# Performance work log

Hardware: AMD Instinct MI355X
Metric: run time of the kernel (lower is better)

The kernel has to match this reference:

```python
import jax, jax.numpy as jnp
import numpy as np

B, P, K, HE, HF = 256, 128, 512, 1024, 512
D = K + HE + 2 * HF  # 2560, MLP input dim
HID = 64


def setup_inputs() -> dict:
    key = jax.random.key(0)
    ks = jax.random.split(key, 6)
    query = jax.random.normal(ks[0], (B, 1, HE), dtype=jnp.float32)
    keys = jax.random.normal(ks[1], (B, P, K), dtype=jnp.float32)
    frameLSTM_h = jax.random.normal(ks[2], (B, 1, 2 * HF), dtype=jnp.float32)
    mask = jax.random.randint(ks[3], (B, P), 0, 2, dtype=jnp.int32)
    mask = mask.at[:, 0].set(1)  # guarantee at least one unmasked player per row
    W1 = jax.random.normal(ks[4], (D, HID), dtype=jnp.float32) / np.float32(np.sqrt(D))
    W2 = jax.random.normal(ks[5], (HID, 1), dtype=jnp.float32) / np.float32(np.sqrt(HID))
    return dict(query=query, keys=keys, frameLSTM_h=frameLSTM_h, mask=mask, W1=W1, W2=W2)


def reference(query, keys, frameLSTM_h, mask, W1, W2):
    # Faithful to: cat([keys, query.repeat, frame.repeat]) @ W1 -> ReLU -> @ W2.
    # The pre-activation is linear, so splitting W1 by row-blocks is exactly the
    # same math without materializing the repeated/concatenated (B,P,D) tensor.
    W1k = W1[:K]            # (K, 64)
    W1q = W1[K:K + HE]      # (HE, 64)
    W1f = W1[K + HE:]       # (2*HF, 64)
    h = jax.nn.relu(
        jnp.einsum('bpk,kh->bph', keys, W1k)
        + jnp.einsum('boe,eh->boh', query, W1q)        # broadcasts over P
        + jnp.einsum('bof,fh->boh', frameLSTM_h, W1f)  # broadcasts over P
    )  # (B, P, 64)
    raw_scores = jnp.einsum('bph,ho->bp', h, W2)  # (B, P)
    raw_scores = jnp.where(mask == 0, -jnp.inf, raw_scores)
    weights = jax.nn.softmax(raw_scores, axis=1)  # (B, P)
    context = jnp.einsum('bp,bpk->bk', weights, keys)[:, None, :]  # (B, 1, K)
    embeddings = jnp.concatenate([context, frameLSTM_h], axis=2)   # (B, 1, K+2*HF)
    return embeddings, weights
```

## Files before the change

### kernel.cpp

```cpp
#include <hip/hip_runtime.h>
#include <hip/hip_bf16.h>
#include <cstdint>
#include <math.h>


typedef __bf16 bf16;
typedef __attribute__((ext_vector_type(8))) __bf16 bf16x8;
typedef __attribute__((ext_vector_type(4))) __bf16 bf16x4;
typedef __attribute__((ext_vector_type(4))) float f32x4;

#define NB 256
#define NP 128
#define NK 512
#define SKLD 520
#define K1_SK_BYTES (64 * SKLD * 2)
#define K1_SMEM (K1_SK_BYTES + 64*4 + 64*4)

__global__ __launch_bounds__(256) void prep_kernel(
    const float* __restrict__ query, const float* __restrict__ frame,
    const float* __restrict__ W1, bf16* __restrict__ w1kt,
    float* __restrict__ proj_part)
{
    const int blk = blockIdx.x;
    const int t = threadIdx.x;
    if (blk < 1024) {
        __shared__ float part[4][64];
        const int b = blk >> 2;
        const int q4 = blk & 3;
        const int h = t & 63;
        const int g = t >> 6;
        const float* src = (q4 < 2 ? query : frame) + (size_t)b * 1024 + (q4 & 1) * 512 + g * 128;
        const float* wrow = W1 + (size_t)(512 + q4 * 512 + g * 128) * 64 + h;
        float acc = 0.f;
#pragma unroll 8
        for (int dd = 0; dd < 128; dd++)
            acc += src[dd] * wrow[(size_t)dd * 64];
        part[g][h] = acc;
        __syncthreads();
        if (t < 64)
            proj_part[((size_t)q4 * NB + b) * 64 + t] =
                part[0][t] + part[1][t] + part[2][t] + part[3][t];
    } else {
        __shared__ float s[32][65];
        const int j = blk - 1024;
        const int k0 = j * 32;
#pragma unroll
        for (int i = 0; i < 8; i++) {
            const int idx = t + 256 * i;
            const int k = idx >> 6, h = idx & 63;
            s[k][h] = W1[(size_t)(k0 + k) * 64 + h];
        }
        __syncthreads();
#pragma unroll
        for (int i = 0; i < 8; i++) {
            const int idx = t + 256 * i;
            const int h = idx >> 5, kk = idx & 31;
            w1kt[(size_t)h * 512 + k0 + kk] = (bf16)s[kk][h];
        }
    }
}

__global__ __launch_bounds__(256, 2) void k1_scores(
    const float* __restrict__ keys, const float* __restrict__ W2,
    const bf16* __restrict__ w1kt, const float* __restrict__ proj_part,
    float* __restrict__ scores_ws)
{
    extern __shared__ char smem[];
    bf16* sk     = (bf16*)smem;
    float* projl = (float*)(smem + K1_SK_BYTES);
    float* w2l   = projl + 64;

    const int b    = blockIdx.x >> 1;
    const int half = blockIdx.x & 1;
    const int t = threadIdx.x;

    if (t < 64)
        projl[t] = proj_part[(size_t)b * 64 + t]
                 + proj_part[((size_t)NB + b) * 64 + t]
                 + proj_part[((size_t)2 * NB + b) * 64 + t]
                 + proj_part[((size_t)3 * NB + b) * 64 + t];
    else if (t < 128) w2l[t - 64] = W2[t - 64];

    const float* kb = keys + (size_t)b * (NP * NK) + (size_t)half * 64 * NK;
    {
        const int rowadd = (t >> 7);
        const int c0 = (t & 127) * 4;
#pragma unroll 8
        for (int i = 0; i < 32; i++) {
            const float4 v = *(const float4*)(kb + (size_t)i * 1024 + t * 4);
            bf16x4 bv;
            bv[0] = (bf16)v.x; bv[1] = (bf16)v.y; bv[2] = (bf16)v.z; bv[3] = (bf16)v.w;
            *(bf16x4*)(sk + (2 * i + rowadd) * SKLD + c0) = bv;
        }
    }
    __syncthreads();

    const int w = t >> 6;
    const int lane = t & 63;
    const int m = lane & 15;
    const int q = lane >> 4;

    const bf16* bbase = w1kt + (size_t)m * 512 + q * 8;
    bf16x8 Bc[4], Bn[4];
#pragma unroll
    for (int nt = 0; nt < 4; nt++) Bc[nt] = *(const bf16x8*)(bbase + nt * 8192);
#pragma unroll
    for (int nt = 0; nt < 4; nt++) Bn[nt] = *(const bf16x8*)(bbase + nt * 8192 + 32);

    f32x4 acc[4];
#pragma unroll
    for (int nt = 0; nt < 4; nt++) acc[nt] = (f32x4){0.f, 0.f, 0.f, 0.f};

#pragma unroll
    for (int kk = 0; kk < 16; kk++) {
        const bf16x8 A = *(const bf16x8*)(sk + (w * 16 + m) * SKLD + kk * 32 + q * 8);
        bf16x8 Bf[4];
#pragma unroll
        for (int nt = 0; nt < 4; nt++) Bf[nt] = Bc[nt];
#pragma unroll
        for (int nt = 0; nt < 4; nt++) Bc[nt] = Bn[nt];
        if (kk < 14) {
#pragma unroll
            for (int nt = 0; nt < 4; nt++)
                Bn[nt] = *(const bf16x8*)(bbase + nt * 8192 + (kk + 2) * 32);
        }
#pragma unroll
        for (int nt = 0; nt < 4; nt++)
            acc[nt] = __builtin_amdgcn_mfma_f32_16x16x32_bf16(A, Bf[nt], acc[nt], 0, 0, 0);
    }

    float pr[4] = {0.f, 0.f, 0.f, 0.f};
#pragma unroll
    for (int nt = 0; nt < 4; nt++) {
        const int h = nt * 16 + m;
        const float pv = projl[h];
        const float wv = w2l[h];
#pragma unroll
        for (int r = 0; r < 4; r++)
            pr[r] += fmaxf(acc[nt][r] + pv, 0.f) * wv;
    }
#pragma unroll
    for (int off = 1; off < 16; off <<= 1) {
#pragma unroll
        for (int r = 0; r < 4; r++) pr[r] += __shfl_xor(pr[r], off);
    }
    if (m == 0) {
        const int base = b * 128 + half * 64 + w * 16 + q * 4;
#pragma unroll
        for (int r = 0; r < 4; r++) scores_ws[base + r] = pr[r];
    }
}

__global__ __launch_bounds__(512) void k2_context(
    const float* __restrict__ keys, const float* __restrict__ frame,
    const int* __restrict__ mask, const float* __restrict__ scores_ws,
    float* __restrict__ out)
{
    __shared__ float s_sc[128];
    __shared__ float s_w[128];
    __shared__ float part[512];

    const int b = blockIdx.x;
    const int t = threadIdx.x;

    if (t < 128) {
        const float raw = scores_ws[b * 128 + t];
        s_sc[t] = (mask[b * 128 + t] == 0) ? -INFINITY : raw;
    }
    __syncthreads();

    if (t < 64) {
        float s0 = s_sc[t], s1 = s_sc[t + 64];
        float mx = fmaxf(s0, s1);
#pragma unroll
        for (int off = 32; off; off >>= 1) mx = fmaxf(mx, __shfl_xor(mx, off));
        float e0 = __expf(s0 - mx), e1 = __expf(s1 - mx);
        float sum = e0 + e1;
#pragma unroll
        for (int off = 32; off; off >>= 1) sum += __shfl_xor(sum, off);
        const float inv = 1.0f / sum;
        s_w[t] = e0 * inv;
        s_w[t + 64] = e1 * inv;
    }
    __syncthreads();

    if (t < 128) out[(size_t)NB * 1536 + b * 128 + t] = s_w[t];

    const int tg = t >> 8;
    const int tc = t & 255;
    const float* kb = keys + (size_t)b * (NP * NK);
    float a0 = 0.f, a1 = 0.f;
#pragma unroll 8
    for (int i = 0; i < 64; i++) {
        const int p = tg * 64 + i;
        const float wv = s_w[p];
        const float2 v = *(const float2*)(kb + (size_t)p * 512 + 2 * tc);
        a0 += wv * v.x;
        a1 += wv * v.y;
    }
    if (tg == 1) {
        part[2 * tc] = a0;
        part[2 * tc + 1] = a1;
    }
    __syncthreads();
    if (tg == 0) {
        out[(size_t)b * 1536 + 2 * tc]     = a0 + part[2 * tc];
        out[(size_t)b * 1536 + 2 * tc + 1] = a1 + part[2 * tc + 1];
    }

    out[(size_t)b * 1536 + 512 + t] = frame[(size_t)b * 1024 + t];
    out[(size_t)b * 1536 + 1024 + t] = frame[(size_t)b * 1024 + 512 + t];
}

extern "C" void kernel_launch(void* const* d_in, const int* in_sizes, int n_in,
                              void* d_out, int out_size, void* d_ws, size_t ws_size,
                              hipStream_t stream) {
    const float* query = (const float*)d_in[0];
    const float* keys  = (const float*)d_in[1];
    const float* frame = (const float*)d_in[2];
    const int*   mask  = (const int*)d_in[3];
    const float* W1    = (const float*)d_in[4];
    const float* W2    = (const float*)d_in[5];
    float* out = (float*)d_out;

    bf16*  w1kt      = (bf16*)d_ws;
    float* proj_part = (float*)((char*)d_ws + (64 << 10));
    float* scores_ws = (float*)((char*)d_ws + (320 << 10));

    hipFuncSetAttribute((const void*)k1_scores,
                        hipFuncAttributeMaxDynamicSharedMemorySize, K1_SMEM);

    prep_kernel<<<1040, 256, 0, stream>>>(query, frame, W1, w1kt, proj_part);
    k1_scores<<<512, 256, K1_SMEM, stream>>>(keys, W2, w1kt, proj_part, scores_ws);
    k2_context<<<256, 512, 0, stream>>>(keys, frame, mask, scores_ws, out);
}
```

Before: 138.3 us.

## Fuse context kernel into score kernel with per-batch inter-block flag handshake

```diff
diff --git a/kernel.cpp b/kernel.cpp
--- a/kernel.cpp
+++ b/kernel.cpp
@@ -14,12 +14,13 @@
 #define NK 512
 #define SKLD 520
 #define K1_SK_BYTES (64 * SKLD * 2)
-#define K1_SMEM (K1_SK_BYTES + 64*4 + 64*4)
+#define K1_SMEM (K1_SK_BYTES + 64*4 + 64*4 + 128*4)
 
 __global__ __launch_bounds__(256) void prep_kernel(
     const float* __restrict__ query, const float* __restrict__ frame,
     const float* __restrict__ W1, bf16* __restrict__ w1kt,
-    float* __restrict__ proj_part)
+    float* __restrict__ proj_part, int* __restrict__ flags,
+    float* __restrict__ out)
 {
     const int blk = blockIdx.x;
     const int t = threadIdx.x;
@@ -50,6 +51,13 @@
             const int k = idx >> 6, h = idx & 63;
             s[k][h] = W1[(size_t)(k0 + k) * 64 + h];
         }
+        if (j == 0) flags[t] = 0;
+#pragma unroll
+        for (int bb = 0; bb < 16; bb++) {
+            const int b = j * 16 + bb;
+            out[(size_t)b * 1536 + t] = 0.f;
+            out[(size_t)b * 1536 + 256 + t] = 0.f;
+        }
         __syncthreads();
 #pragma unroll
         for (int i = 0; i < 8; i++) {
@@ -60,15 +68,18 @@
     }
 }
 
-__global__ __launch_bounds__(256, 2) void k1_scores(
-    const float* __restrict__ keys, const float* __restrict__ W2,
+__global__ __launch_bounds__(256, 2) void k1_attn(
+    const float* __restrict__ keys, const float* __restrict__ frame,
+    const int* __restrict__ mask, const float* __restrict__ W2,
     const bf16* __restrict__ w1kt, const float* __restrict__ proj_part,
-    float* __restrict__ scores_ws)
+    float* __restrict__ scores_ws, int* __restrict__ flags,
+    float* __restrict__ out)
 {
     extern __shared__ char smem[];
     bf16* sk     = (bf16*)smem;
     float* projl = (float*)(smem + K1_SK_BYTES);
     float* w2l   = projl + 64;
+    float* wts   = w2l + 64;
 
     const int b    = blockIdx.x >> 1;
     const int half = blockIdx.x & 1;
@@ -83,7 +94,7 @@
 
     const float* kb = keys + (size_t)b * (NP * NK) + (size_t)half * 64 * NK;
     {
-        const int rowadd = (t >> 7);
+        const int rowadd = t >> 7;
         const int c0 = (t & 127) * 4;
 #pragma unroll 8
         for (int i = 0; i < 32; i++) {
@@ -147,30 +158,29 @@
     if (m == 0) {
         const int base = b * 128 + half * 64 + w * 16 + q * 4;
 #pragma unroll
-        for (int r = 0; r < 4; r++) scores_ws[base + r] = pr[r];
-    }
-}
-
-__global__ __launch_bounds__(512) void k2_context(
-    const float* __restrict__ keys, const float* __restrict__ frame,
-    const int* __restrict__ mask, const float* __restrict__ scores_ws,
-    float* __restrict__ out)
-{
-    __shared__ float s_sc[128];
-    __shared__ float s_w[128];
-    __shared__ float part[512];
-
-    const int b = blockIdx.x;
-    const int t = threadIdx.x;
+        for (int r = 0; r < 4; r++)
+            __hip_atomic_store(&scores_ws[base + r], pr[r],
+                               __ATOMIC_RELAXED, __HIP_MEMORY_SCOPE_AGENT);
+    }
+    __threadfence();
+    __syncthreads();
+
+    if (t == 0) {
+        atomicAdd(&flags[b], 1);
+        while (__hip_atomic_load(&flags[b], __ATOMIC_ACQUIRE,
+                                 __HIP_MEMORY_SCOPE_AGENT) < 2)
+            __builtin_amdgcn_s_sleep(1);
+    }
+    __syncthreads();
 
     if (t < 128) {
-        const float raw = scores_ws[b * 128 + t];
-        s_sc[t] = (mask[b * 128 + t] == 0) ? -INFINITY : raw;
-    }
-    __syncthreads();
-
-    if (t < 64) {
-        float s0 = s_sc[t], s1 = s_sc[t + 64];
+        const float raw = __hip_atomic_load(&scores_ws[b * 128 + t],
+                                            __ATOMIC_RELAXED, __HIP_MEMORY_SCOPE_AGENT);
+        wts[t] = (mask[b * 128 + t] == 0) ? -INFINITY : raw;
+    }
+    __syncthreads();
+    if (w == 0) {
+        float s0 = wts[lane], s1 = wts[lane + 64];
         float mx = fmaxf(s0, s1);
 #pragma unroll
         for (int off = 32; off; off >>= 1) mx = fmaxf(mx, __shfl_xor(mx, off));
@@ -179,37 +189,32 @@
 #pragma unroll
         for (int off = 32; off; off >>= 1) sum += __shfl_xor(sum, off);
         const float inv = 1.0f / sum;
-        s_w[t] = e0 * inv;
-        s_w[t + 64] = e1 * inv;
-    }
-    __syncthreads();
-
-    if (t < 128) out[(size_t)NB * 1536 + b * 128 + t] = s_w[t];
-
-    const int tg = t >> 8;
-    const int tc = t & 255;
-    const float* kb = keys + (size_t)b * (NP * NK);
-    float a0 = 0.f, a1 = 0.f;
+        wts[lane] = e0 * inv;
+        wts[lane + 64] = e1 * inv;
+    }
+    __syncthreads();
+
+    if (half == 0 && t < 128)
+        out[(size_t)NB * 1536 + b * 128 + t] = wts[t];
+
+    {
+        float a0 = 0.f, a1 = 0.f;
+        const int c = 2 * t;
 #pragma unroll 8
-    for (int i = 0; i < 64; i++) {
-        const int p = tg * 64 + i;
-        const float wv = s_w[p];
-        const float2 v = *(const float2*)(kb + (size_t)p * 512 + 2 * tc);
-        a0 += wv * v.x;
-        a1 += wv * v.y;
-    }
-    if (tg == 1) {
-        part[2 * tc] = a0;
-        part[2 * tc + 1] = a1;
-    }
-    __syncthreads();
-    if (tg == 0) {
-        out[(size_t)b * 1536 + 2 * tc]     = a0 + part[2 * tc];
-        out[(size_t)b * 1536 + 2 * tc + 1] = a1 + part[2 * tc + 1];
-    }
-
-    out[(size_t)b * 1536 + 512 + t] = frame[(size_t)b * 1024 + t];
-    out[(size_t)b * 1536 + 1024 + t] = frame[(size_t)b * 1024 + 512 + t];
+        for (int r = 0; r < 64; r++) {
+            const float wv = wts[half * 64 + r];
+            const uint32_t uv = *(const uint32_t*)(sk + r * SKLD + c);
+            a0 += wv * __uint_as_float(uv << 16);
+            a1 += wv * __uint_as_float(uv & 0xffff0000u);
+        }
+        atomicAdd(&out[(size_t)b * 1536 + c], a0);
+        atomicAdd(&out[(size_t)b * 1536 + c + 1], a1);
+    }
+
+    if (half == 1) {
+        const float4 fv = *(const float4*)(frame + (size_t)b * 1024 + t * 4);
+        *(float4*)(out + (size_t)b * 1536 + 512 + t * 4) = fv;
+    }
 }
 
 extern "C" void kernel_launch(void* const* d_in, const int* in_sizes, int n_in,
@@ -225,12 +230,13 @@
 
     bf16*  w1kt      = (bf16*)d_ws;
     float* proj_part = (float*)((char*)d_ws + (64 << 10));
-    float* scores_ws = (float*)((char*)d_ws + (320 << 10));
-
-    hipFuncSetAttribute((const void*)k1_scores,
+    int*   flags     = (int*)((char*)d_ws + (320 << 10));
+    float* scores_ws = (float*)((char*)d_ws + (324 << 10));
+
+    hipFuncSetAttribute((const void*)k1_attn,
                         hipFuncAttributeMaxDynamicSharedMemorySize, K1_SMEM);
 
-    prep_kernel<<<1040, 256, 0, stream>>>(query, frame, W1, w1kt, proj_part);
-    k1_scores<<<512, 256, K1_SMEM, stream>>>(keys, W2, w1kt, proj_part, scores_ws);
-    k2_context<<<256, 512, 0, stream>>>(keys, frame, mask, scores_ws, out);
+    prep_kernel<<<1040, 256, 0, stream>>>(query, frame, W1, w1kt, proj_part, flags, out);
+    k1_attn<<<512, 256, K1_SMEM, stream>>>(keys, frame, mask, W2, w1kt, proj_part,
+                                           scores_ws, flags, out);
 }
```

After: 159.2 us. 15.2% more time.
